# Kernel optimization log

Measured on AMD Instinct MI355X. Metric: run time of the kernel, lower is better.

## Reference

```python
import jax, jax.numpy as jnp
import numpy as np

B, T, D = 64, 2048, 512


def setup_inputs() -> dict:
    key = jax.random.key(0)
    ks = jax.random.split(key, 6)
    lim_tau = 1.0 / np.sqrt(2 * D)  # torch Linear default init bound
    lim_mem = 1.0 / np.sqrt(D)
    return {
        "x": jax.random.normal(ks[0], (B, T, D), dtype=jnp.float32),
        "tau_w": jax.random.uniform(ks[1], (D, 2 * D), jnp.float32, -lim_tau, lim_tau),
        "tau_b": jax.random.uniform(ks[2], (D,), jnp.float32, -lim_tau, lim_tau),
        "mem_w": jax.random.uniform(ks[3], (D, D), jnp.float32, -lim_mem, lim_mem),
        "mem_b": jax.random.uniform(ks[4], (D,), jnp.float32, -lim_mem, lim_mem),
        "log_thresh": jnp.zeros((D,), jnp.float32),
    }


def reference(x, tau_w, tau_b, mem_w, mem_b, log_thresh):
    b, t, d = x.shape
    thr = jax.nn.sigmoid(log_thresh)  # [D]

    def step(carry, xt):
        v, tau = carry  # each [B, D]
        # liquid time-constant gate: sigmoid(Linear([xt, tau]))
        tau = jax.nn.sigmoid(jnp.concatenate([xt, tau], axis=-1) @ tau_w.T + tau_b)
        alpha = jnp.exp(-1.0 / (tau + 1e-6))
        v = alpha * v + (1.0 - alpha) * (xt @ mem_w.T + mem_b)
        s = (v >= thr).astype(x.dtype)  # spike
        v = v * (1.0 - s)  # hard reset
        return (v, tau), s

    x_tbd = jnp.swapaxes(x, 0, 1)  # [T, B, D] for scan
    init = (jnp.zeros((b, d), x.dtype), jnp.ones((b, d), x.dtype))
    (v, tau), spikes = jax.lax.scan(step, init, x_tbd)
    return jnp.swapaxes(spikes, 0, 1), tau, v  # [B,T,D], [B,D], [B,D]
```

## Files before the change

kernel.cpp:

```cpp
#include <hip/hip_runtime.h>
#include <math.h>

#define B_ 64
#define T_ 2048
#define D_ 512
#define BT_ (B_ * T_)
#define XWORDS (B_ * D_)

typedef unsigned long long u64;

__global__ void prep_weights(const float* __restrict__ tau_w,
                             const float* __restrict__ mem_w,
                             float* __restrict__ Wcat,
                             float* __restrict__ WTh) {
    int idx = blockIdx.x * 256 + threadIdx.x;
    {
        int k = idx >> 10, j = idx & 1023;
        float v = (j < 512) ? tau_w[j * 1024 + k] : mem_w[(j - 512) * 512 + k];
        Wcat[idx] = v;
    }
    if (idx < 512 * 512) {
        int k = idx >> 9, d = idx & 511;
        WTh[idx] = tau_w[d * 1024 + 512 + k];
    }
}

__global__ __launch_bounds__(256, 2)
void gemm_xw(const float* __restrict__ X, const float* __restrict__ Wc,
             const float* __restrict__ tau_b, const float* __restrict__ mem_b,
             float* __restrict__ Aout, float* __restrict__ Mout) {
    __shared__ __align__(16) float As[16][128];
    __shared__ __align__(16) float Bs[16][128];
    const int bn = blockIdx.x;
    const int bm = blockIdx.y;
    const int tid = threadIdx.x;
    const int tm = (tid >> 4) << 3;
    const int tn = (tid & 15) << 3;
    const int m0 = bm * 128, n0 = bn * 128;

    const float4* X4 = (const float4*)X;
    const float4* Wc4 = (const float4*)Wc;

    float acc[8][8];
#pragma unroll
    for (int i = 0; i < 8; i++)
#pragma unroll
        for (int j = 0; j < 8; j++) acc[i][j] = 0.0f;

    const int ar = tid >> 1;
    const int ac2 = (tid & 1) * 2;
    const int bkr = tid >> 4;
    const int bc = (tid & 15) * 2;

    for (int kt = 0; kt < 512; kt += 16) {
        float4 av0 = X4[(m0 + ar) * 128 + (kt >> 2) + ac2];
        float4 av1 = X4[(m0 + ar) * 128 + (kt >> 2) + ac2 + 1];
        float4 bv0 = Wc4[(kt + bkr) * 256 + bn * 32 + bc];
        float4 bv1 = Wc4[(kt + bkr) * 256 + bn * 32 + bc + 1];
        __syncthreads();
        As[ac2 * 4 + 0][ar] = av0.x;
        As[ac2 * 4 + 1][ar] = av0.y;
        As[ac2 * 4 + 2][ar] = av0.z;
        As[ac2 * 4 + 3][ar] = av0.w;
        As[ac2 * 4 + 4][ar] = av1.x;
        As[ac2 * 4 + 5][ar] = av1.y;
        As[ac2 * 4 + 6][ar] = av1.z;
        As[ac2 * 4 + 7][ar] = av1.w;
        *(float4*)&Bs[bkr][bc * 4] = bv0;
        *(float4*)&Bs[bkr][bc * 4 + 4] = bv1;
        __syncthreads();
#pragma unroll
        for (int kk = 0; kk < 16; kk++) {
            float4 a0 = *(const float4*)&As[kk][tm];
            float4 a1 = *(const float4*)&As[kk][tm + 4];
            float4 b0 = *(const float4*)&Bs[kk][tn];
            float4 b1 = *(const float4*)&Bs[kk][tn + 4];
            float av[8] = {a0.x, a0.y, a0.z, a0.w, a1.x, a1.y, a1.z, a1.w};
            float bv[8] = {b0.x, b0.y, b0.z, b0.w, b1.x, b1.y, b1.z, b1.w};
#pragma unroll
            for (int i = 0; i < 8; i++)
#pragma unroll
                for (int j = 0; j < 8; j++)
                    acc[i][j] = fmaf(av[i], bv[j], acc[i][j]);
        }
    }

    const bool isA = (bn < 4);
    float* Cout = isA ? Aout : Mout;
    const float* bias = isA ? tau_b : mem_b;
    const int ncol0 = (isA ? n0 : n0 - 512) + tn;
    float bj[8];
#pragma unroll
    for (int j = 0; j < 8; j++) bj[j] = bias[ncol0 + j];
#pragma unroll
    for (int i = 0; i < 8; i++) {
        size_t off = (size_t)(m0 + tm + i) * 512 + ncol0;
        float4 o0, o1;
        o0.x = acc[i][0] + bj[0]; o0.y = acc[i][1] + bj[1];
        o0.z = acc[i][2] + bj[2]; o0.w = acc[i][3] + bj[3];
        o1.x = acc[i][4] + bj[4]; o1.y = acc[i][5] + bj[5];
        o1.z = acc[i][6] + bj[6]; o1.w = acc[i][7] + bj[7];
        *(float4*)&Cout[off] = o0;
        *(float4*)&Cout[off + 4] = o1;
    }
}

__global__ void init_sync(u64* __restrict__ xchg, int* __restrict__ ctr) {
    int idx = blockIdx.x * 256 + threadIdx.x;
    if (idx < 2 * XWORDS) xchg[idx] = (idx < XWORDS) ? 0x3F800000ull : 0ull;
    if (idx < 16) ctr[idx] = 0;
}

__global__ __launch_bounds__(512)
__attribute__((amdgpu_waves_per_eu(2, 2)))
void scan_reg(const float* __restrict__ WTh,
              const float* __restrict__ Mm,
              const float* __restrict__ log_thresh,
              float* __restrict__ AmOut,
              float* __restrict__ OutTail,
              u64* __restrict__ xchg,
              int* __restrict__ ctr) {
    __shared__ __align__(16) float part[2][8][64];
    __shared__ __align__(16) float tau_sm[2][64];
    __shared__ int role_s;
    __shared__ float4 pad_lds[7168];

    const int tid = threadIdx.x;
    if (tid == 9999) ((volatile float*)pad_lds)[0] = 1.f;

    if (tid == 0) {
        unsigned xcd;
        asm volatile("s_getreg_b32 %0, hwreg(HW_REG_XCC_ID)" : "=s"(xcd));
        xcd &= 7;
        int rank = atomicAdd(&ctr[xcd], 1) & 31;
        role_s = ((rank & 7) << 8) | ((int)xcd * 4 + (rank >> 3));
    }
    __syncthreads();
    const int sg = role_s >> 8;
    const int bp = role_s & 255;

    const int ws = tid >> 6;
    const int lane = tid & 63;
    const bool self = (ws == sg);

    const float* wcol = WTh + sg * 64 + lane;
    float4 w[16];
#pragma unroll
    for (int q4 = 0; q4 < 16; q4++) {
        const int k0 = ws * 64 + q4 * 4;
        w[q4].x = wcol[(size_t)(k0 + 0) * 512];
        w[q4].y = wcol[(size_t)(k0 + 1) * 512];
        w[q4].z = wcol[(size_t)(k0 + 2) * 512];
        w[q4].w = wcol[(size_t)(k0 + 3) * 512];
    }

    const int eb = tid >> 6;
    const int ech = tid & 63;
    const int gch = sg * 64 + ech;
    float thr = 0.f, v = 0.f, tau_keep = 0.f;
    if (tid < 128) thr = 1.0f / (1.0f + expf(-log_thresh[gch]));
    size_t abase = ((size_t)(bp * 2 + eb) * T_) * D_ + gch;

    if (tid < 128) tau_sm[eb][ech] = 1.0f;

    float a_pf = 0.f, m_pf = 0.f;
    if (tid < 128) { a_pf = AmOut[abase]; m_pf = Mm[abase]; }
    __syncthreads();

    for (int c = 1; c <= T_; c++) {
        float a_nx = 0.f, m_nx = 0.f;
        if (tid < 128) {
            size_t nx = (c < T_) ? abase + D_ : abase;
            a_nx = AmOut[nx]; m_nx = Mm[nx];
        }

        float t0f, t1f;
        if (!self) {
            const u64* s0 = xchg + (size_t)((c - 1) & 1) * XWORDS
                                 + (size_t)(bp * 2) * 512 + ws * 64 + lane;
            const u64* s1 = s0 + 512;
            const unsigned tgt = (unsigned)(c - 1);
            u64 v0, v1;
            int guard = 0;
            do {
                v0 = __hip_atomic_load(s0, __ATOMIC_RELAXED,
                                       __HIP_MEMORY_SCOPE_AGENT);
                v1 = __hip_atomic_load(s1, __ATOMIC_RELAXED,
                                       __HIP_MEMORY_SCOPE_AGENT);
            } while ((((unsigned)(v0 >> 32) < tgt) |
                      ((unsigned)(v1 >> 32) < tgt)) && ++guard < (1 << 22));
            t0f = __uint_as_float((unsigned)v0);
            t1f = __uint_as_float((unsigned)v1);
        } else {
            t0f = tau_sm[0][lane];
            t1f = tau_sm[1][lane];
        }
        const int t0i = __float_as_int(t0f);
        const int t1i = __float_as_int(t1f);

        float acc0 = 0.f, acc1 = 0.f;
#pragma unroll
        for (int q4 = 0; q4 < 16; q4++) {
#pragma unroll
            for (int j = 0; j < 4; j++) {
                const int kk = q4 * 4 + j;
                const float wv = (j == 0) ? w[q4].x : (j == 1) ? w[q4].y
                               : (j == 2) ? w[q4].z : w[q4].w;
                float ta = __uint_as_float(
                    (unsigned)__builtin_amdgcn_readlane(t0i, kk));
                float tb = __uint_as_float(
                    (unsigned)__builtin_amdgcn_readlane(t1i, kk));
                acc0 = fmaf(ta, wv, acc0);
                acc1 = fmaf(tb, wv, acc1);
            }
        }
        part[0][ws][lane] = acc0;
        part[1][ws][lane] = acc1;
        __syncthreads();

        if (tid < 128) {
            float sum = 0.f;
#pragma unroll
            for (int j = 0; j < 8; j++) sum += part[eb][j][ech];
            float pre = sum + a_pf;
            float tau = 1.0f / (1.0f + expf(-pre));
            float alpha = expf(-1.0f / (tau + 1e-6f));
            v = alpha * v + (1.0f - alpha) * m_pf;
            float s = (v >= thr) ? 1.0f : 0.0f;
            AmOut[abase] = s;
            v = v * (1.0f - s);
            tau_keep = tau;
            tau_sm[eb][ech] = tau;
            u64 pack = ((u64)(unsigned)c << 32) | (u64)__float_as_uint(tau);
            __hip_atomic_store(&xchg[(size_t)(c & 1) * XWORDS
                                     + (bp * 2 + eb) * 512 + gch],
                               pack, __ATOMIC_RELAXED, __HIP_MEMORY_SCOPE_AGENT);
            abase += D_;
            a_pf = a_nx; m_pf = m_nx;
        }
        __syncthreads();
    }

    if (tid < 128) {
        const size_t batch = bp * 2 + eb;
        OutTail[(size_t)BT_ * D_ + batch * D_ + gch] = tau_keep;
        OutTail[(size_t)BT_ * D_ + (size_t)B_ * D_ + batch * D_ + gch] = v;
    }
}

extern "C" void kernel_launch(void* const* d_in, const int* in_sizes, int n_in,
                              void* d_out, int out_size, void* d_ws, size_t ws_size,
                              hipStream_t stream) {
    (void)in_sizes; (void)n_in; (void)out_size; (void)ws_size;
    const float* x          = (const float*)d_in[0];
    const float* tau_w      = (const float*)d_in[1];
    const float* tau_b      = (const float*)d_in[2];
    const float* mem_w      = (const float*)d_in[3];
    const float* mem_b      = (const float*)d_in[4];
    const float* log_thresh = (const float*)d_in[5];
    float* out = (float*)d_out;

    float* Wcat = (float*)d_ws;
    float* WTh  = Wcat + 512 * 1024;
    float* Mout = WTh + 512 * 512;
    u64* xchg = (u64*)d_ws;
    int* ctr  = (int*)((char*)d_ws + 2 * XWORDS * sizeof(u64));

    float* Aout = out;

    prep_weights<<<2048, 256, 0, stream>>>(tau_w, mem_w, Wcat, WTh);
    gemm_xw<<<dim3(8, 1024), 256, 0, stream>>>(x, Wcat, tau_b, mem_b, Aout, Mout);
    init_sync<<<256, 256, 0, stream>>>(xchg, ctr);

    const float* WThc = WTh;
    const float* Mmc  = Mout;
    const float* ltc  = log_thresh;
    float* outp = out;
    u64* xchgp = xchg;
    int* ctrp = ctr;
    void* args[7] = {(void*)&WThc, (void*)&Mmc, (void*)&ltc,
                     (void*)&Aout, (void*)&outp, (void*)&xchgp, (void*)&ctrp};
    hipLaunchCooperativeKernel((const void*)scan_reg, dim3(256), dim3(512),
                               args, 0, stream);
}
```

Measured before the change: 5.861 ms.

## Move recurrent weights to LDS, double-buffer partials, drop second barrier per step

Recurrent weight slices now sit in LDS instead of registers, replacing the LDS padding array. The partial-sum buffer is double-buffered by step parity so the trailing __syncthreads per timestep can be removed. The tau exchange is published before the alpha/spike math, and every wave, including its own group, now reads tau from the global exchange rather than a local shared copy. This shortens the serial critical path per step, at the cost of an LDS read per weight vector and polling global memory for local data.

Measured after the change: 6.037 ms. 1.03x slower.

```diff
diff --git a/kernel.cpp b/kernel.cpp
--- a/kernel.cpp
+++ b/kernel.cpp
@@ -113,20 +113,18 @@
 
 __global__ __launch_bounds__(512)
 __attribute__((amdgpu_waves_per_eu(2, 2)))
-void scan_reg(const float* __restrict__ WTh,
-              const float* __restrict__ Mm,
-              const float* __restrict__ log_thresh,
-              float* __restrict__ AmOut,
-              float* __restrict__ OutTail,
-              u64* __restrict__ xchg,
-              int* __restrict__ ctr) {
-    __shared__ __align__(16) float part[2][8][64];
-    __shared__ __align__(16) float tau_sm[2][64];
+void scan_rl(const float* __restrict__ WTh,
+             const float* __restrict__ Mm,
+             const float* __restrict__ log_thresh,
+             float* __restrict__ AmOut,
+             float* __restrict__ OutTail,
+             u64* __restrict__ xchg,
+             int* __restrict__ ctr) {
+    __shared__ __align__(16) float4 w_lds[8192];
+    __shared__ __align__(16) float part[2][2][8][64];
     __shared__ int role_s;
-    __shared__ float4 pad_lds[7168];
 
     const int tid = threadIdx.x;
-    if (tid == 9999) ((volatile float*)pad_lds)[0] = 1.f;
 
     if (tid == 0) {
         unsigned xcd;
@@ -139,20 +137,19 @@
     const int sg = role_s >> 8;
     const int bp = role_s & 255;
 
+    {
+        const int ch = tid & 63;
+        const int kr8 = tid >> 6;
+        float* wl = (float*)w_lds;
+        for (int i = 0; i < 64; i++) {
+            int krow = i * 8 + kr8;
+            wl[(krow >> 2) * 256 + ch * 4 + (krow & 3)] =
+                WTh[krow * 512 + sg * 64 + ch];
+        }
+    }
+
     const int ws = tid >> 6;
     const int lane = tid & 63;
-    const bool self = (ws == sg);
-
-    const float* wcol = WTh + sg * 64 + lane;
-    float4 w[16];
-#pragma unroll
-    for (int q4 = 0; q4 < 16; q4++) {
-        const int k0 = ws * 64 + q4 * 4;
-        w[q4].x = wcol[(size_t)(k0 + 0) * 512];
-        w[q4].y = wcol[(size_t)(k0 + 1) * 512];
-        w[q4].z = wcol[(size_t)(k0 + 2) * 512];
-        w[q4].w = wcol[(size_t)(k0 + 3) * 512];
-    }
 
     const int eb = tid >> 6;
     const int ech = tid & 63;
@@ -161,8 +158,6 @@
     if (tid < 128) thr = 1.0f / (1.0f + expf(-log_thresh[gch]));
     size_t abase = ((size_t)(bp * 2 + eb) * T_) * D_ + gch;
 
-    if (tid < 128) tau_sm[eb][ech] = 1.0f;
-
     float a_pf = 0.f, m_pf = 0.f;
     if (tid < 128) { a_pf = AmOut[abase]; m_pf = Mm[abase]; }
     __syncthreads();
@@ -174,71 +169,63 @@
             a_nx = AmOut[nx]; m_nx = Mm[nx];
         }
 
-        float t0f, t1f;
-        if (!self) {
-            const u64* s0 = xchg + (size_t)((c - 1) & 1) * XWORDS
-                                 + (size_t)(bp * 2) * 512 + ws * 64 + lane;
-            const u64* s1 = s0 + 512;
-            const unsigned tgt = (unsigned)(c - 1);
-            u64 v0, v1;
-            int guard = 0;
-            do {
-                v0 = __hip_atomic_load(s0, __ATOMIC_RELAXED,
-                                       __HIP_MEMORY_SCOPE_AGENT);
-                v1 = __hip_atomic_load(s1, __ATOMIC_RELAXED,
-                                       __HIP_MEMORY_SCOPE_AGENT);
-            } while ((((unsigned)(v0 >> 32) < tgt) |
-                      ((unsigned)(v1 >> 32) < tgt)) && ++guard < (1 << 22));
-            t0f = __uint_as_float((unsigned)v0);
-            t1f = __uint_as_float((unsigned)v1);
-        } else {
-            t0f = tau_sm[0][lane];
-            t1f = tau_sm[1][lane];
-        }
-        const int t0i = __float_as_int(t0f);
-        const int t1i = __float_as_int(t1f);
+        const u64* s0 = xchg + (size_t)((c - 1) & 1) * XWORDS
+                             + (size_t)(bp * 2) * 512 + ws * 64 + lane;
+        const u64* s1 = s0 + 512;
+        const unsigned tgt = (unsigned)(c - 1);
+        u64 v0, v1;
+        int guard = 0;
+        do {
+            v0 = __hip_atomic_load(s0, __ATOMIC_RELAXED,
+                                   __HIP_MEMORY_SCOPE_AGENT);
+            v1 = __hip_atomic_load(s1, __ATOMIC_RELAXED,
+                                   __HIP_MEMORY_SCOPE_AGENT);
+        } while ((((unsigned)(v0 >> 32) < tgt) |
+                  ((unsigned)(v1 >> 32) < tgt)) && ++guard < (1 << 22));
+        const int t0i = (int)(unsigned)v0;
+        const int t1i = (int)(unsigned)v1;
 
         float acc0 = 0.f, acc1 = 0.f;
 #pragma unroll
         for (int q4 = 0; q4 < 16; q4++) {
+            float4 wv = w_lds[(ws * 16 + q4) * 64 + lane];
 #pragma unroll
             for (int j = 0; j < 4; j++) {
                 const int kk = q4 * 4 + j;
-                const float wv = (j == 0) ? w[q4].x : (j == 1) ? w[q4].y
-                               : (j == 2) ? w[q4].z : w[q4].w;
+                const float wj = (j == 0) ? wv.x : (j == 1) ? wv.y
+                               : (j == 2) ? wv.z : wv.w;
                 float ta = __uint_as_float(
                     (unsigned)__builtin_amdgcn_readlane(t0i, kk));
                 float tb = __uint_as_float(
                     (unsigned)__builtin_amdgcn_readlane(t1i, kk));
-                acc0 = fmaf(ta, wv, acc0);
-                acc1 = fmaf(tb, wv, acc1);
+                acc0 = fmaf(ta, wj, acc0);
+                acc1 = fmaf(tb, wj, acc1);
             }
         }
-        part[0][ws][lane] = acc0;
-        part[1][ws][lane] = acc1;
+        const int par = c & 1;
+        part[par][0][ws][lane] = acc0;
+        part[par][1][ws][lane] = acc1;
         __syncthreads();
 
         if (tid < 128) {
             float sum = 0.f;
 #pragma unroll
-            for (int j = 0; j < 8; j++) sum += part[eb][j][ech];
+            for (int j = 0; j < 8; j++) sum += part[par][eb][j][ech];
             float pre = sum + a_pf;
             float tau = 1.0f / (1.0f + expf(-pre));
+            u64 pack = ((u64)(unsigned)c << 32) | (u64)__float_as_uint(tau);
+            __hip_atomic_store(&xchg[(size_t)(c & 1) * XWORDS
+                                     + (bp * 2 + eb) * 512 + gch],
+                               pack, __ATOMIC_RELAXED, __HIP_MEMORY_SCOPE_AGENT);
             float alpha = expf(-1.0f / (tau + 1e-6f));
             v = alpha * v + (1.0f - alpha) * m_pf;
             float s = (v >= thr) ? 1.0f : 0.0f;
             AmOut[abase] = s;
             v = v * (1.0f - s);
             tau_keep = tau;
-            tau_sm[eb][ech] = tau;
-            u64 pack = ((u64)(unsigned)c << 32) | (u64)__float_as_uint(tau);
-            __hip_atomic_store(&xchg[(size_t)(c & 1) * XWORDS
-                                     + (bp * 2 + eb) * 512 + gch],
-                               pack, __ATOMIC_RELAXED, __HIP_MEMORY_SCOPE_AGENT);
             abase += D_;
             a_pf = a_nx; m_pf = m_nx;
         }
-        __syncthreads();
     }
 
     if (tid < 128) {
@@ -280,6 +267,6 @@
     int* ctrp = ctr;
     void* args[7] = {(void*)&WThc, (void*)&Mmc, (void*)&ltc,
                      (void*)&Aout, (void*)&outp, (void*)&xchgp, (void*)&ctrp};
-    hipLaunchCooperativeKernel((const void*)scan_reg, dim3(256), dim3(512),
+    hipLaunchCooperativeKernel((const void*)scan_rl, dim3(256), dim3(512),
                                args, 0, stream);
 }
```
